# Optimization experiments

Measured on AMD Instinct MI355X. Metric: run time of the kernel, lower is better.

## Reference

```python
import jax, jax.numpy as jnp
import numpy as np

H, HD, RD = 16, 128, 64          # n_heads, head_dim, rope_dim
CD = HD - RD                      # content_dim = 64
THETA = 10000.0


def apply_rope(x, cos, sin):
    # x: [B,H,T,RD]; cos/sin: [T,RD//2] broadcast over B,H
    d = x.shape[-1] // 2
    x1, x2 = x[..., :d], x[..., d:]
    return jnp.concatenate([x1 * cos - x2 * sin, x1 * sin + x2 * cos], axis=-1)


def setup_inputs() -> dict:
    key = jax.random.key(0)
    ks = jax.random.split(key, 9)
    d_model, q_rank, d_latent = 2048, 512, 512
    B, T = 2, 2048
    s = 0.02
    return {
        "x": jax.random.normal(ks[0], (B, T, d_model), dtype=jnp.float32),
        "Wq_down": jax.random.normal(ks[1], (d_model, q_rank), dtype=jnp.float32) * s,
        "Wq_up": jax.random.normal(ks[2], (q_rank, H * CD), dtype=jnp.float32) * s,
        "Wq_rope": jax.random.normal(ks[3], (d_model, H * RD), dtype=jnp.float32) * s,
        "Wkv_down": jax.random.normal(ks[4], (d_model, d_latent), dtype=jnp.float32) * s,
        "Wk_up": jax.random.normal(ks[5], (d_latent, H * CD), dtype=jnp.float32) * s,
        "Wv_up": jax.random.normal(ks[6], (d_latent, H * HD), dtype=jnp.float32) * s,
        "Wk_rope": jax.random.normal(ks[7], (d_model, H * RD), dtype=jnp.float32) * s,
        "Wo": jax.random.normal(ks[8], (H * HD, d_model), dtype=jnp.float32) * s,
    }


def reference(x, Wq_down, Wq_up, Wq_rope, Wkv_down, Wk_up, Wv_up, Wk_rope, Wo):
    B, T, _ = x.shape

    # low-rank projections
    q_content = (x @ Wq_down) @ Wq_up            # [B,T,H*CD]
    q_pos = x @ Wq_rope                          # [B,T,H*RD]
    kv_latent = x @ Wkv_down                     # [B,T,d_latent]
    k_content = kv_latent @ Wk_up                # [B,T,H*CD]
    k_pos = x @ Wk_rope                          # [B,T,H*RD]
    v = kv_latent @ Wv_up                        # [B,T,H*HD]

    def split_heads(t, d):
        return t.reshape(B, T, H, d).transpose(0, 2, 1, 3)  # [B,H,T,d]

    q_content = split_heads(q_content, CD)
    q_pos = split_heads(q_pos, RD)
    k_content = split_heads(k_content, CD)
    k_pos = split_heads(k_pos, RD)
    v = split_heads(v, HD)

    # rotary tables: [T, RD//2]
    inv_freq = 1.0 / (THETA ** (jnp.arange(0, RD, 2, dtype=jnp.float32) / RD))
    freqs = jnp.arange(T, dtype=jnp.float32)[:, None] * inv_freq[None, :]
    cos, sin = jnp.cos(freqs), jnp.sin(freqs)

    q_pos = apply_rope(q_pos, cos, sin)
    k_pos = apply_rope(k_pos, cos, sin)

    q = jnp.concatenate([q_content, q_pos], axis=-1)  # [B,H,T,HD]
    k = jnp.concatenate([k_content, k_pos], axis=-1)  # [B,H,T,HD]

    # causal SDPA, scale = 1/sqrt(head_dim)
    scale = 1.0 / jnp.sqrt(jnp.asarray(HD, dtype=q.dtype))
    scores = jnp.einsum("bhqd,bhkd->bhqk", q, k) * scale
    causal = jnp.tril(jnp.ones((T, T), dtype=bool))
    scores = jnp.where(causal, scores, jnp.finfo(scores.dtype).min)
    attn = jax.nn.softmax(scores, axis=-1)
    out = jnp.einsum("bhqk,bhkd->bhqd", attn, v)      # [B,H,T,HD]

    out = out.transpose(0, 2, 1, 3).reshape(B, T, H * HD)
    return out @ Wo
```

## Files before the change

kernel.cpp:

```cpp
#include <hip/hip_runtime.h>
#include <hip/hip_bf16.h>
#include <stdint.h>
#include <math.h>

#define H_ 16
#define HD_ 128
#define RD_ 64
#define CD_ 64
#define DM_ 2048
#define QR_ 512
#define DL_ 512
#define B_ 2
#define T_ 2048
#define M_TOT (B_*T_)

typedef __attribute__((ext_vector_type(8))) short short8;
typedef __attribute__((ext_vector_type(4))) float f32x4;
typedef __attribute__((ext_vector_type(16))) float f32x16;

__device__ __forceinline__ unsigned short f2b_hw(float f){
  __hip_bfloat16 h = __float2bfloat16(f);
  union { __hip_bfloat16 h; unsigned short u; } c; c.h = h; return c.u;
}
__device__ __forceinline__ float b2f(unsigned short b){
  union { unsigned u; float f; } a; a.u = ((unsigned)b) << 16;
  return a.f;
}
__device__ __forceinline__ unsigned pack2(float lo, float hi){
  __hip_bfloat162 h2 = __float22bfloat162_rn(make_float2(lo, hi));
  union { __hip_bfloat162 h; unsigned u; } c; c.h = h2; return c.u;
}

#define GLOAD16(g, l) __builtin_amdgcn_global_load_lds( \
    (__attribute__((address_space(1))) void*)(g), \
    (__attribute__((address_space(3))) void*)(l), 16, 0, 0)

__global__ void cast_f32_bf16(const float* __restrict__ src,
                              unsigned short* __restrict__ dst, int n){
  int i = (blockIdx.x * blockDim.x + threadIdx.x) * 4;
  if (i < n){
    float4 v = *(const float4*)(src + i);
    ushort4 o;
    o.x = f2b_hw(v.x); o.y = f2b_hw(v.y); o.z = f2b_hw(v.z); o.w = f2b_hw(v.w);
    *(ushort4*)(dst + i) = o;
  }
}

struct TTe { const float* src; unsigned short* dst; int K, N, blk0; };
struct TT8 { TTe e[8]; };

__global__ void transpose_cast8(TT8 tab){
  __shared__ float tile[32][33];
  int bid = blockIdx.x;
  const float* src = tab.e[0].src;
  unsigned short* dst = tab.e[0].dst;
  int K = tab.e[0].K, N = tab.e[0].N, loc = bid;
  #pragma unroll
  for (int j = 1; j < 8; j++){
    if (bid >= tab.e[j].blk0){
      src = tab.e[j].src; dst = tab.e[j].dst;
      K = tab.e[j].K; N = tab.e[j].N; loc = bid - tab.e[j].blk0;
    }
  }
  int cols = N / 32;
  int n0 = (loc % cols) * 32, k0 = (loc / cols) * 32;
  int tx = threadIdx.x, ty = threadIdx.y;
  #pragma unroll
  for (int r = ty; r < 32; r += 8)
    tile[r][tx] = src[(size_t)(k0 + r) * N + n0 + tx];
  __syncthreads();
  #pragma unroll
  for (int r = ty; r < 32; r += 8)
    dst[(size_t)(n0 + r) * K + k0 + tx] = f2b_hw(tile[tx][r]);
}

template<int MODE>
__global__ __launch_bounds__(256) void gemm_bt(
    const unsigned short* __restrict__ A, int lda,
    const unsigned short* __restrict__ Bt,
    void* __restrict__ Cv, void* __restrict__ Cv2, int ldc, int N, int K)
{
  __shared__ unsigned short As[128 * 32];
  __shared__ unsigned short Bs[128 * 32];
  int tid = threadIdx.x;

  int gx = gridDim.x;
  int nwg = gx * gridDim.y;
  int lin = blockIdx.x + gx * blockIdx.y;
  int q8 = nwg >> 3;
  int nl = (lin & 7) * q8 + (lin >> 3);
  int m0 = (nl / gx) * 128, n0 = (nl % gx) * 128;

  int lane = tid & 63, w = tid >> 6;
  int wr = (w >> 1) * 64, wc = (w & 1) * 64;
  int mr = lane & 15, kg = lane >> 4;

  const unsigned short* Ag = A  + (size_t)(m0 + (tid >> 2)) * lda + ((tid & 3) << 3);
  const unsigned short* Bg = Bt + (size_t)(n0 + (tid >> 2)) * K + ((tid & 3) << 3);

  f32x4 acc[4][4];
  #pragma unroll
  for (int i = 0; i < 4; i++)
    #pragma unroll
    for (int j = 0; j < 4; j++)
      acc[i][j] = (f32x4){0.f, 0.f, 0.f, 0.f};

  for (int k0 = 0; k0 < K; k0 += 32) {
    #pragma unroll
    for (int j = 0; j < 2; j++) {
      GLOAD16(Ag + (size_t)j * 64 * lda, &As[j * 2048 + tid * 8]);
      GLOAD16(Bg + (size_t)j * 64 * K, &Bs[j * 2048 + tid * 8]);
    }
    Ag += 32; Bg += 32;
    __syncthreads();
    short8 af[4], bf[4];
    #pragma unroll
    for (int i = 0; i < 4; i++)
      af[i] = *(const short8*)&As[(wr + i * 16 + mr) * 32 + kg * 8];
    #pragma unroll
    for (int j = 0; j < 4; j++)
      bf[j] = *(const short8*)&Bs[(wc + j * 16 + mr) * 32 + kg * 8];
    __builtin_amdgcn_s_setprio(1);
    #pragma unroll
    for (int i = 0; i < 4; i++)
      #pragma unroll
      for (int j = 0; j < 4; j++)
        acc[i][j] = __builtin_amdgcn_mfma_f32_16x16x32_bf16(af[i], bf[j], acc[i][j], 0, 0, 0);
    __builtin_amdgcn_s_setprio(0);
    __syncthreads();
  }

  if (MODE == 1) {
    float* C = (float*)Cv;
    #pragma unroll
    for (int i = 0; i < 4; i++)
      #pragma unroll
      for (int j = 0; j < 4; j++)
        #pragma unroll
        for (int r = 0; r < 4; r++) {
          int row = m0 + wr + i * 16 + kg * 4 + r;
          int col = n0 + wc + j * 16 + mr;
          C[(size_t)row * ldc + col] = acc[i][j][r];
        }
  } else if (MODE == 0) {
    unsigned short* C = (unsigned short*)Cv;
    #pragma unroll
    for (int i = 0; i < 4; i++)
      #pragma unroll
      for (int j = 0; j < 4; j++)
        #pragma unroll
        for (int r = 0; r < 4; r++) {
          int row = m0 + wr + i * 16 + kg * 4 + r;
          int col = n0 + wc + j * 16 + mr;
          C[(size_t)row * ldc + col] = f2b_hw(acc[i][j][r]);
        }
  } else if (MODE == 2) {
    unsigned short* qhp = (unsigned short*)Cv;
    #pragma unroll
    for (int i = 0; i < 4; i++)
      #pragma unroll
      for (int j = 0; j < 4; j++) {
        int colb = n0 + wc + j * 16 + mr;
        int h = colb >> 6, d = colb & 63;
        #pragma unroll
        for (int r = 0; r < 4; r++) {
          int gr = m0 + wr + i * 16 + kg * 4 + r;
          size_t idx = ((size_t)((gr >> 11) * H_ + h) * T_ + (gr & (T_-1))) * 128 + d;
          qhp[idx] = f2b_hw(acc[i][j][r]);
        }
      }
  } else {
    unsigned short* khp = (unsigned short*)Cv;
    unsigned short* vtp = (unsigned short*)Cv2;
    if (n0 < 1024) {
      #pragma unroll
      for (int i = 0; i < 4; i++)
        #pragma unroll
        for (int j = 0; j < 4; j++) {
          int colb = n0 + wc + j * 16 + mr;
          int h = colb >> 6, d = colb & 63;
          #pragma unroll
          for (int r = 0; r < 4; r++) {
            int gr = m0 + wr + i * 16 + kg * 4 + r;
            size_t idx = ((size_t)((gr >> 11) * H_ + h) * T_ + (gr & (T_-1))) * 128 + d;
            khp[idx] = f2b_hw(acc[i][j][r]);
          }
        }
    } else {
      #pragma unroll
      for (int i = 0; i < 4; i++)
        #pragma unroll
        for (int j = 0; j < 4; j++) {
          int c2 = n0 + wc + j * 16 + mr - 1024;
          int h = c2 >> 7, d = c2 & 127;
          int gr0 = m0 + wr + i * 16 + kg * 4;
          int b = gr0 >> 11, t0 = gr0 & (T_-1);
          ushort4 o;
          o.x = f2b_hw(acc[i][j][0]); o.y = f2b_hw(acc[i][j][1]);
          o.z = f2b_hw(acc[i][j][2]); o.w = f2b_hw(acc[i][j][3]);
          size_t idx = ((size_t)(b * H_ + h) * 128 + d) * T_ + t0;
          *(ushort4*)&vtp[idx] = o;
        }
    }
  }
}

__global__ void rope_fill(const unsigned short* __restrict__ projall,
                          unsigned short* __restrict__ qh,
                          unsigned short* __restrict__ kh){
  int row = blockIdx.x * 8 + threadIdx.y;
  int j = threadIdx.x;
  int bh = row >> 11;
  int t  = row & (T_ - 1);
  int b = bh >> 4, h = bh & 15;
  size_t srow = (size_t)b * T_ + t;
  const unsigned short* qp = projall + srow * 3072 + 1024 + h * 64;
  const unsigned short* kp = qp + 1024;
  float invf = exp2f(-(float)j * 0.4152410118750f);
  float f = (float)t * invf;
  float s, c;
  sincosf(f, &s, &c);
  float qx1 = b2f(qp[j]), qx2 = b2f(qp[j + 32]);
  float kx1 = b2f(kp[j]), kx2 = b2f(kp[j + 32]);
  size_t dst = ((size_t)bh * T_ + t) * 128 + 64;
  qh[dst + j]      = f2b_hw(qx1 * c - qx2 * s);
  qh[dst + j + 32] = f2b_hw(qx1 * s + qx2 * c);
  kh[dst + j]      = f2b_hw(kx1 * c - kx2 * s);
  kh[dst + j + 32] = f2b_hw(kx1 * s + kx2 * c);
}

__global__ __launch_bounds__(256, 2) void attn_fwd5(
    const unsigned short* __restrict__ qh,
    const unsigned short* __restrict__ kh,
    const unsigned short* __restrict__ vt,
    unsigned short* __restrict__ ao)
{
  __shared__ __align__(16) unsigned short lds[4 * 8192];

  const int tid  = threadIdx.x;
  const int lane = tid & 63, w = tid >> 6;
  const int l31  = lane & 31, hi = lane >> 5;

  int lin = blockIdx.x + 16 * blockIdx.y;
  int r8 = lin & 7, s = lin >> 3;
  int bh = r8 * 4 + (s >> 4);
  int j  = s & 15;
  int qt = ((s >> 5) & 1) ? (15 - j) : j;

  const int b  = bh >> 4, hd = bh & 15;
  const int q0    = qt * 128;
  const int q0w   = q0 + w * 32;
  const int qg    = q0w + l31;
  const int qmaxw = q0w + 31;
  const int nt    = 2 * qt + 2;

  const unsigned short* Qg = qh + (size_t)bh * T_ * 128;
  const unsigned short* Kg = kh + (size_t)bh * T_ * 128;
  const unsigned short* Vg = vt + (size_t)bh * 128 * T_;

  short8 qf[8];
  #pragma unroll
  for (int kc = 0; kc < 8; kc++)
    qf[kc] = *(const short8*)&Qg[(size_t)qg * 128 + kc * 16 + hi * 8];

  f32x16 accO[4];
  #pragma unroll
  for (int sb = 0; sb < 4; sb++)
    #pragma unroll
    for (int r = 0; r < 16; r++) accO[sb][r] = 0.f;

  float m = -1e30f, lsum = 0.f;
  const float SC = 0.12751743f;

  int krow[4], kwof[4], vrow[4], vwof[4];
  #pragma unroll
  for (int jj = 0; jj < 4; jj++){
    int r_ = (w * 4 + jj) * 4 + (lane >> 4);
    krow[jj] = r_;
    kwof[jj] = r_ * 128 + ((((lane & 15) * 16) ^ ((r_ & 7) << 4)) >> 1);
    int d_ = (w * 4 + jj) * 8 + (lane >> 3);
    vrow[jj] = d_;
    vwof[jj] = d_ * 64 + ((((lane & 7) * 16) ^ ((d_ & 7) << 4)) >> 1);
  }
  const int kcol = (lane & 15) * 8;
  const int vcol = (lane & 7) * 8;

  uint4 kst[4], vst[4];

#define REG_LOAD(kvt) do {                                                    \
    int kv0s = (kvt) * 64;                                                    \
    _Pragma("unroll")                                                         \
    for (int j_ = 0; j_ < 4; j_++) {                                          \
      kst[j_] = *(const uint4*)&Kg[(size_t)(kv0s + krow[j_]) * 128 + kcol];   \
      vst[j_] = *(const uint4*)&Vg[(size_t)vrow[j_] * T_ + kv0s + vcol];      \
    }                                                                         \
  } while (0)

#define DS_WRITE(bufi) do {                                                   \
    unsigned short* ksb_ = lds + (bufi) * 8192;                               \
    unsigned short* vsb_ = lds + 16384 + (bufi) * 8192;                       \
    _Pragma("unroll")                                                         \
    for (int j_ = 0; j_ < 4; j_++) {                                          \
      *(uint4*)&ksb_[kwof[j_]] = kst[j_];                                     \
      *(uint4*)&vsb_[vwof[j_]] = vst[j_];                                     \
    }                                                                         \
  } while (0)

  REG_LOAD(0);
  DS_WRITE(0);
  if (nt > 1) REG_LOAD(1);
  asm volatile("s_waitcnt lgkmcnt(0)" ::: "memory");
  __builtin_amdgcn_s_barrier();
  __builtin_amdgcn_sched_barrier(0);

  for (int t = 0; t < nt; t++) {
    const int cur = t & 1;
    if (t + 1 < nt) DS_WRITE(cur ^ 1);
    if (t + 2 < nt) REG_LOAD(t + 2);
    const int kv0 = t * 64;
    if (kv0 <= qmaxw) {
      const unsigned short* Kb = lds + cur * 8192;
      const unsigned short* Vb = lds + 16384 + cur * 8192;

      f32x16 sa0, sa1;
      #pragma unroll
      for (int r = 0; r < 16; r++) { sa0[r] = 0.f; sa1[r] = 0.f; }
      __builtin_amdgcn_s_setprio(1);
      #pragma unroll
      for (int kc = 0; kc < 8; kc++) {
        int co = (kc * 32 + hi * 16);
        int r0 = l31;
        short8 kf0 = *(const short8*)&Kb[r0 * 128 + ((co ^ ((r0 & 7) << 4)) >> 1)];
        sa0 = __builtin_amdgcn_mfma_f32_32x32x16_bf16(kf0, qf[kc], sa0, 0, 0, 0);
        int r1 = 32 + l31;
        short8 kf1 = *(const short8*)&Kb[r1 * 128 + ((co ^ ((r1 & 7) << 4)) >> 1)];
        sa1 = __builtin_amdgcn_mfma_f32_32x32x16_bf16(kf1, qf[kc], sa1, 0, 0, 0);
      }
      __builtin_amdgcn_s_setprio(0);

      float p0[16], p1[16];
      float pmax = -1e30f;
      bool needMask = (kv0 + 63 > q0w);
      if (needMask) {
        #pragma unroll
        for (int r = 0; r < 16; r++) {
          int crow = (r & 3) + 8 * (r >> 2) + 4 * hi;
          float v0 = sa0[r] * SC;
          float v1 = sa1[r] * SC;
          if (kv0 + crow > qg)      v0 = -1e30f;
          if (kv0 + 32 + crow > qg) v1 = -1e30f;
          p0[r] = v0; p1[r] = v1;
          pmax = fmaxf(pmax, fmaxf(v0, v1));
        }
      } else {
        #pragma unroll
        for (int r = 0; r < 16; r++) {
          float v0 = sa0[r] * SC;
          float v1 = sa1[r] * SC;
          p0[r] = v0; p1[r] = v1;
          pmax = fmaxf(pmax, fmaxf(v0, v1));
        }
      }
      pmax = fmaxf(pmax, __shfl_xor(pmax, 32, 64));
      if (!__all(pmax <= m + 8.f)) {
        float mn  = fmaxf(m, pmax);
        float fac = exp2f(m - mn);
        m = mn;
        lsum *= fac;
        #pragma unroll
        for (int sb = 0; sb < 4; sb++)
          #pragma unroll
          for (int r = 0; r < 16; r++) accO[sb][r] *= fac;
      }
      float ls = 0.f;
      #pragma unroll
      for (int r = 0; r < 16; r++) {
        p0[r] = exp2f(p0[r] - m);
        p1[r] = exp2f(p1[r] - m);
        ls += p0[r] + p1[r];
      }
      ls += __shfl_xor(ls, 32, 64);
      lsum += ls;

      #pragma unroll
      for (int kc2 = 0; kc2 < 4; kc2++) {
        unsigned A01, A23, B01, B23;
        if (kc2 == 0) { A01 = pack2(p0[0], p0[1]);  A23 = pack2(p0[2], p0[3]);
                        B01 = pack2(p0[4], p0[5]);  B23 = pack2(p0[6], p0[7]); }
        else if (kc2 == 1) { A01 = pack2(p0[8], p0[9]);   A23 = pack2(p0[10], p0[11]);
                             B01 = pack2(p0[12], p0[13]); B23 = pack2(p0[14], p0[15]); }
        else if (kc2 == 2) { A01 = pack2(p1[0], p1[1]);  A23 = pack2(p1[2], p1[3]);
                             B01 = pack2(p1[4], p1[5]);  B23 = pack2(p1[6], p1[7]); }
        else { A01 = pack2(p1[8], p1[9]);   A23 = pack2(p1[10], p1[11]);
               B01 = pack2(p1[12], p1[13]); B23 = pack2(p1[14], p1[15]); }
        asm("v_permlane32_swap_b32 %0, %1" : "+v"(A01), "+v"(B01));
        asm("v_permlane32_swap_b32 %0, %1" : "+v"(A23), "+v"(B23));
        union { unsigned u[4]; short8 v; } pk;
        pk.u[0] = A01; pk.u[1] = A23; pk.u[2] = B01; pk.u[3] = B23;
        short8 pa = pk.v;
        __builtin_amdgcn_s_setprio(1);
        #pragma unroll
        for (int sb = 0; sb < 4; sb++) {
          int d = sb * 32 + l31;
          short8 vf = *(const short8*)&Vb[d * 64 + (((kc2 * 32 + hi * 16) ^ ((d & 7) << 4)) >> 1)];
          accO[sb] = __builtin_amdgcn_mfma_f32_32x32x16_bf16(vf, pa, accO[sb], 0, 0, 0);
        }
        __builtin_amdgcn_s_setprio(0);
      }
    }
    __builtin_amdgcn_sched_barrier(0);
    asm volatile("s_waitcnt lgkmcnt(0)" ::: "memory");
    __builtin_amdgcn_s_barrier();
    __builtin_amdgcn_sched_barrier(0);
  }

  float rl = 1.0f / lsum;
  size_t orow = ((size_t)b * T_ + qg) * (H_*HD_) + hd * 128;
  #pragma unroll
  for (int sb = 0; sb < 4; sb++)
    #pragma unroll
    for (int g = 0; g < 4; g++) {
      ushort4 o;
      o.x = f2b_hw(accO[sb][4 * g + 0] * rl);
      o.y = f2b_hw(accO[sb][4 * g + 1] * rl);
      o.z = f2b_hw(accO[sb][4 * g + 2] * rl);
      o.w = f2b_hw(accO[sb][4 * g + 3] * rl);
      *(ushort4*)&ao[orow + sb * 32 + 8 * g + 4 * hi] = o;
    }
#undef REG_LOAD
#undef DS_WRITE
}

extern "C" void kernel_launch(void* const* d_in, const int* in_sizes, int n_in,
                              void* d_out, int out_size, void* d_ws, size_t ws_size,
                              hipStream_t stream)
{
  (void)in_sizes; (void)n_in; (void)out_size; (void)ws_size;
  const float* x        = (const float*)d_in[0];
  const float* Wq_down  = (const float*)d_in[1];
  const float* Wq_up    = (const float*)d_in[2];
  const float* Wq_rope  = (const float*)d_in[3];
  const float* Wkv_down = (const float*)d_in[4];
  const float* Wk_up    = (const float*)d_in[5];
  const float* Wv_up    = (const float*)d_in[6];
  const float* Wk_rope  = (const float*)d_in[7];
  const float* Wo       = (const float*)d_in[8];

  char* ws = (char*)d_ws;
  unsigned short* xb      = (unsigned short*)(ws + 0);
  unsigned short* Wdall   = (unsigned short*)(ws + 16777216);
  unsigned short* WquT    = (unsigned short*)(ws + 29360128);
  unsigned short* WkcvT   = (unsigned short*)(ws + 30408704);
  unsigned short* WoT     = (unsigned short*)(ws + 33554432);
  unsigned short* projall = (unsigned short*)(ws + 41943040);
  unsigned short* qh      = (unsigned short*)(ws + 67108864);
  unsigned short* kh      = (unsigned short*)(ws + 83886080);
  unsigned short* vt      = (unsigned short*)(ws + 100663296);
  unsigned short* ao      = projall;

  dim3 tb(32, 8);

  cast_f32_bf16<<<(M_TOT * DM_ / 4 + 255) / 256, 256, 0, stream>>>(x, xb, M_TOT * DM_);

  TT8 tab;
  int blk = 0;
  tab.e[0] = { Wq_down,  Wdall,               DM_, QR_,     blk }; blk += (QR_/32)*(DM_/32);
  tab.e[1] = { Wkv_down, Wdall + 512*2048,    DM_, DL_,     blk }; blk += (DL_/32)*(DM_/32);
  tab.e[2] = { Wq_rope,  Wdall + 1024*2048,   DM_, H_*RD_,  blk }; blk += (H_*RD_/32)*(DM_/32);
  tab.e[3] = { Wk_rope,  Wdall + 2048*2048,   DM_, H_*RD_,  blk }; blk += (H_*RD_/32)*(DM_/32);
  tab.e[4] = { Wq_up,    WquT,                QR_, H_*CD_,  blk }; blk += (H_*CD_/32)*(QR_/32);
  tab.e[5] = { Wk_up,    WkcvT,               DL_, H_*CD_,  blk }; blk += (H_*CD_/32)*(DL_/32);
  tab.e[6] = { Wv_up,    WkcvT + 1024*512,    DL_, H_*HD_,  blk }; blk += (H_*HD_/32)*(DL_/32);
  tab.e[7] = { Wo,       WoT,                 H_*HD_, DM_,  blk }; blk += (DM_/32)*(H_*HD_/32);
  transpose_cast8<<<blk, tb, 0, stream>>>(tab);

  gemm_bt<0><<<dim3(3072/128, M_TOT/128), 256, 0, stream>>>(xb, DM_, Wdall, projall, nullptr, 3072, 3072, DM_);
  gemm_bt<2><<<dim3(1024/128, M_TOT/128), 256, 0, stream>>>(projall, 3072, WquT, qh, nullptr, 0, 1024, QR_);
  gemm_bt<3><<<dim3(3072/128, M_TOT/128), 256, 0, stream>>>(projall + 512, 3072, WkcvT, kh, vt, 0, 3072, DL_);
  rope_fill<<<dim3(B_*H_*T_/8), dim3(32, 8), 0, stream>>>(projall, qh, kh);

  attn_fwd5<<<dim3(16, 32), 256, 0, stream>>>(qh, kh, vt, ao);

  gemm_bt<1><<<dim3(DM_/128, M_TOT/128), 256, 0, stream>>>(ao, 2048, WoT, d_out, nullptr, DM_, DM_, H_*HD_);
}
```

Baseline: 341.5 us.

## Fuse RoPE into down-projection GEMM epilogue and simplify attention block mapping

The first GEMM's epilogue now applies rotary embedding directly to the q_pos/k_pos columns and writes them into the head-major qh/kh buffers. This removes the separate rope_fill kernel and lets projall shrink to only the latent part (ldc 1024). It relies on each 128-column tile holding both halves of each 64-wide head, which holds for the wc/jp indexing used. The attention kernel drops the swizzled block-to-(bh,qt) mapping in favour of a plain blockIdx mapping with reversed q-tiles for half the heads, and writes output to a separate buffer. That mapping change may alter L2 locality and load balance. The epilogue adds sincos work inside the GEMM.

Result: slower. 348.8 us (+2.1%).

```diff
diff --git a/kernel.cpp b/kernel.cpp
--- a/kernel.cpp
+++ b/kernel.cpp
@@ -78,7 +78,8 @@
 __global__ __launch_bounds__(256) void gemm_bt(
     const unsigned short* __restrict__ A, int lda,
     const unsigned short* __restrict__ Bt,
-    void* __restrict__ Cv, void* __restrict__ Cv2, int ldc, int N, int K)
+    void* __restrict__ Cv, void* __restrict__ Cv2, void* __restrict__ Cv3,
+    int ldc, int N, int K)
 {
   __shared__ unsigned short As[128 * 32];
   __shared__ unsigned short Bs[128 * 32];
@@ -169,7 +170,7 @@
           qhp[idx] = f2b_hw(acc[i][j][r]);
         }
       }
-  } else {
+  } else if (MODE == 3) {
     unsigned short* khp = (unsigned short*)Cv;
     unsigned short* vtp = (unsigned short*)Cv2;
     if (n0 < 1024) {
@@ -202,34 +203,49 @@
           *(ushort4*)&vtp[idx] = o;
         }
     }
-  }
-}
-
-__global__ void rope_fill(const unsigned short* __restrict__ projall,
-                          unsigned short* __restrict__ qh,
-                          unsigned short* __restrict__ kh){
-  int row = blockIdx.x * 8 + threadIdx.y;
-  int j = threadIdx.x;
-  int bh = row >> 11;
-  int t  = row & (T_ - 1);
-  int b = bh >> 4, h = bh & 15;
-  size_t srow = (size_t)b * T_ + t;
-  const unsigned short* qp = projall + srow * 3072 + 1024 + h * 64;
-  const unsigned short* kp = qp + 1024;
-  float invf = exp2f(-(float)j * 0.4152410118750f);
-  float f = (float)t * invf;
-  float s, c;
-  sincosf(f, &s, &c);
-  float qx1 = b2f(qp[j]), qx2 = b2f(qp[j + 32]);
-  float kx1 = b2f(kp[j]), kx2 = b2f(kp[j + 32]);
-  size_t dst = ((size_t)bh * T_ + t) * 128 + 64;
-  qh[dst + j]      = f2b_hw(qx1 * c - qx2 * s);
-  qh[dst + j + 32] = f2b_hw(qx1 * s + qx2 * c);
-  kh[dst + j]      = f2b_hw(kx1 * c - kx2 * s);
-  kh[dst + j + 32] = f2b_hw(kx1 * s + kx2 * c);
-}
-
-__global__ __launch_bounds__(256, 2) void attn_fwd5(
+  } else {
+    if (n0 < 1024) {
+      unsigned short* C = (unsigned short*)Cv;
+      #pragma unroll
+      for (int i = 0; i < 4; i++)
+        #pragma unroll
+        for (int j = 0; j < 4; j++)
+          #pragma unroll
+          for (int r = 0; r < 4; r++) {
+            int row = m0 + wr + i * 16 + kg * 4 + r;
+            int col = n0 + wc + j * 16 + mr;
+            C[(size_t)row * ldc + col] = f2b_hw(acc[i][j][r]);
+          }
+    } else {
+      const bool isq = (n0 < 2048);
+      unsigned short* dst = (unsigned short*)(isq ? Cv2 : Cv3);
+      int cbase = n0 - (isq ? 1024 : 2048);
+      #pragma unroll
+      for (int jp = 0; jp < 2; jp++) {
+        int colA = wc + jp * 16 + mr;
+        int cA = cbase + colA;
+        int h = cA >> 6, jr = cA & 63;
+        float invf = exp2f(-(float)jr * 0.4152410118750f);
+        #pragma unroll
+        for (int i = 0; i < 4; i++)
+          #pragma unroll
+          for (int r = 0; r < 4; r++) {
+            int gr = m0 + wr + i * 16 + kg * 4 + r;
+            int t = gr & (T_ - 1);
+            float fr = (float)t * invf;
+            float s_, c_;
+            sincosf(fr, &s_, &c_);
+            float x1 = acc[i][jp][r], x2 = acc[i][jp + 2][r];
+            size_t base = ((size_t)((gr >> 11) * H_ + h) * T_ + t) * 128 + 64;
+            dst[base + jr]      = f2b_hw(x1 * c_ - x2 * s_);
+            dst[base + jr + 32] = f2b_hw(x1 * s_ + x2 * c_);
+          }
+      }
+    }
+  }
+}
+
+__global__ __launch_bounds__(256, 2) void attn_fwd7(
     const unsigned short* __restrict__ qh,
     const unsigned short* __restrict__ kh,
     const unsigned short* __restrict__ vt,
@@ -240,16 +256,11 @@
   const int tid  = threadIdx.x;
   const int lane = tid & 63, w = tid >> 6;
   const int l31  = lane & 31, hi = lane >> 5;
-
-  int lin = blockIdx.x + 16 * blockIdx.y;
-  int r8 = lin & 7, s = lin >> 3;
-  int bh = r8 * 4 + (s >> 4);
-  int j  = s & 15;
-  int qt = ((s >> 5) & 1) ? (15 - j) : j;
-
+  const int bh = blockIdx.y;
   const int b  = bh >> 4, hd = bh & 15;
-  const int q0    = qt * 128;
-  const int q0w   = q0 + w * 32;
+  int qt = blockIdx.x;
+  if (bh >= 16) qt = 15 - qt;
+  const int q0w   = qt * 128 + w * 32;
   const int qg    = q0w + l31;
   const int qmaxw = q0w + 31;
   const int nt    = 2 * qt + 2;
@@ -456,7 +467,7 @@
   unsigned short* qh      = (unsigned short*)(ws + 67108864);
   unsigned short* kh      = (unsigned short*)(ws + 83886080);
   unsigned short* vt      = (unsigned short*)(ws + 100663296);
-  unsigned short* ao      = projall;
+  unsigned short* ao      = (unsigned short*)(ws + 117440512);
 
   dim3 tb(32, 8);
 
@@ -474,12 +485,11 @@
   tab.e[7] = { Wo,       WoT,                 H_*HD_, DM_,  blk }; blk += (DM_/32)*(H_*HD_/32);
   transpose_cast8<<<blk, tb, 0, stream>>>(tab);
 
-  gemm_bt<0><<<dim3(3072/128, M_TOT/128), 256, 0, stream>>>(xb, DM_, Wdall, projall, nullptr, 3072, 3072, DM_);
-  gemm_bt<2><<<dim3(1024/128, M_TOT/128), 256, 0, stream>>>(projall, 3072, WquT, qh, nullptr, 0, 1024, QR_);
-  gemm_bt<3><<<dim3(3072/128, M_TOT/128), 256, 0, stream>>>(projall + 512, 3072, WkcvT, kh, vt, 0, 3072, DL_);
-  rope_fill<<<dim3(B_*H_*T_/8), dim3(32, 8), 0, stream>>>(projall, qh, kh);
-
-  attn_fwd5<<<dim3(16, 32), 256, 0, stream>>>(qh, kh, vt, ao);
-
-  gemm_bt<1><<<dim3(DM_/128, M_TOT/128), 256, 0, stream>>>(ao, 2048, WoT, d_out, nullptr, DM_, DM_, H_*HD_);
-}
+  gemm_bt<4><<<dim3(3072/128, M_TOT/128), 256, 0, stream>>>(xb, DM_, Wdall, projall, qh, kh, 1024, 3072, DM_);
+  gemm_bt<2><<<dim3(1024/128, M_TOT/128), 256, 0, stream>>>(projall, 1024, WquT, qh, nullptr, nullptr, 0, 1024, QR_);
+  gemm_bt<3><<<dim3(3072/128, M_TOT/128), 256, 0, stream>>>(projall + 512, 1024, WkcvT, kh, vt, nullptr, 0, 3072, DL_);
+
+  attn_fwd7<<<dim3(16, 32), 256, 0, stream>>>(qh, kh, vt, ao);
+
+  gemm_bt<1><<<dim3(DM_/128, M_TOT/128), 256, 0, stream>>>(ao, 2048, WoT, d_out, nullptr, nullptr, DM_, DM_, H_*HD_);
+}
```
